# Kernel tuning notes

Measured on AMD Instinct MI355X. Metric: run time of the kernel, lower is better.

Reference implementation:

```python
import jax, jax.numpy as jnp
import numpy as np

DEPTH = 9            # perfect binary tree depth (root=level 0, leaves=level DEPTH)
N_TREES = 128
H = 256              # h_size == x_size (ndata['h'] init uses x_size)
NPT = 2 ** (DEPTH + 1) - 1   # 1023 nodes per tree
N = N_TREES * NPT            # 130944 total nodes


def _levels():
    """Static per-level (node, left-child, right-child) global index arrays."""
    base = np.arange(N_TREES, dtype=np.int64)[:, None] * NPT
    out = []
    for l in range(DEPTH + 1):
        loc = np.arange(2 ** l - 1, 2 ** (l + 1) - 1, dtype=np.int64)
        nodes = (base + loc[None, :]).reshape(-1)
        if l < DEPTH:
            cl = (base + (2 * loc + 1)[None, :]).reshape(-1)
            cr = (base + (2 * loc + 2)[None, :]).reshape(-1)
        else:
            cl = cr = None
        out.append((jnp.asarray(nodes),
                    None if cl is None else jnp.asarray(cl),
                    None if cr is None else jnp.asarray(cr)))
    return out


def setup_inputs() -> dict:
    key = jax.random.key(0)
    ks = jax.random.split(key, 10)
    s = lambda d: 1.0 / np.sqrt(d)
    return {
        "wordid": jax.random.randint(ks[0], (N,), 0, 32000),
        "mask":   jax.random.randint(ks[1], (N,), 0, 2),
        "emb":    jax.random.normal(ks[2], (32000, H), jnp.float32) * 0.02,
        "W_iou":  jax.random.normal(ks[3], (H, 3 * H), jnp.float32) * s(H),
        "U_iou":  jax.random.normal(ks[4], (2 * H, 3 * H), jnp.float32) * s(2 * H),
        "U_f_w":  jax.random.normal(ks[5], (2 * H, 2 * H), jnp.float32) * s(2 * H),
        "U_f_b":  jax.random.normal(ks[6], (2 * H,), jnp.float32) * 0.01,
        "b_iou":  jax.random.normal(ks[7], (3 * H,), jnp.float32) * 0.01,
        "lin_w":  jax.random.normal(ks[8], (H, 4), jnp.float32) * s(H),
        "lin_b":  jax.random.normal(ks[9], (4,), jnp.float32) * 0.01,
    }


def _apply_node(iou, b_iou, c_in, mh_in):
    i, o, u = jnp.split(iou + b_iou, 3, axis=1)
    i, o, u = jax.nn.sigmoid(i), jax.nn.sigmoid(o), jnp.tanh(u)
    c = i * u + c_in
    h = o * jnp.tanh(c)
    return h, c, jnp.maximum(h, mh_in)


def reference(wordid, mask, emb, W_iou, U_iou, U_f_w, U_f_b, b_iou, lin_w, lin_b):
    levels = _levels()
    x = emb[wordid * mask]                                  # [N, H]
    iou0 = (x @ W_iou) * mask[:, None].astype(x.dtype)      # leaf/pre-set iou [N, 3H]

    h = jnp.zeros((N, H), x.dtype)
    c = jnp.zeros((N, H), x.dtype)
    mh = jnp.zeros((N, H), x.dtype)

    # leaves: no incoming messages -> apply with preset iou, c=0, max_h=0
    li, _, _ = levels[DEPTH]
    hh, cc, mm = _apply_node(iou0[li], b_iou, 0.0, 0.0)
    h, c, mh = h.at[li].set(hh), c.at[li].set(cc), mh.at[li].set(mm)

    # internal levels, bottom-up (DGL prop_nodes_topo)
    for l in range(DEPTH - 1, -1, -1):
        ni, cl, cr = levels[l]
        h_cat = jnp.concatenate([h[cl], h[cr]], axis=1)     # [M, 2H]
        f = jax.nn.sigmoid(h_cat @ U_f_w + U_f_b)           # [M, 2H]
        fl, fr = jnp.split(f, 2, axis=1)
        c_red = fl * c[cl] + fr * c[cr]
        mh_red = jnp.maximum(mh[cl], mh[cr])
        iou = h_cat @ U_iou                                  # overwrites preset iou
        hh, cc, mm = _apply_node(iou, b_iou, c_red, mh_red)
        h, c, mh = h.at[ni].set(hh), c.at[ni].set(cc), mh.at[ni].set(mm)

    return (h + mh) @ lin_w + lin_b                         # logits [N, num_classes]
```

## Files before the change

kernel.cpp:

```cpp
#include <hip/hip_runtime.h>
#include <hip/hip_bf16.h>


#define NTREES 128
#define NPT    1023
#define HS     256
#define NNODES (NTREES * NPT)
#define NL     (NTREES * 512)

typedef __hip_bfloat16 bf16;
typedef unsigned short us8 __attribute__((ext_vector_type(8)));
typedef unsigned short us4 __attribute__((ext_vector_type(4)));
typedef short bf16x8 __attribute__((ext_vector_type(8)));
typedef float f32x4 __attribute__((ext_vector_type(4)));

typedef __attribute__((address_space(1))) const void gvoid;
typedef __attribute__((address_space(3))) void svoid;
#define GLD16(gp, lp) \
    __builtin_amdgcn_global_load_lds((gvoid*)(gp), (svoid*)(lp), 16, 0, 0)

__device__ __forceinline__ float bits2f(unsigned short b) {
    return __uint_as_float(((unsigned)b) << 16);
}
__device__ __forceinline__ unsigned short f2bits(float x) {
    bf16 h = __float2bfloat16(x);
    return *reinterpret_cast<unsigned short*>(&h);
}
__device__ __forceinline__ float fsigm(float x) {
    return __builtin_amdgcn_rcpf(1.0f + __expf(-x));
}
__device__ __forceinline__ float ftanh(float x) {
    return 1.0f - 2.0f * __builtin_amdgcn_rcpf(1.0f + __expf(2.0f * x));
}

#define WT_ELEMS (768 * 256)
#define UT_ELEMS (1280 * 512)

__global__ __launch_bounds__(256) void prep_w(
    const float* __restrict__ W_iou, const float* __restrict__ U_f_w,
    const float* __restrict__ U_iou, bf16* __restrict__ Wt, bf16* __restrict__ Ut)
{
    const int i = blockIdx.x * 256 + threadIdx.x;
    if (i < WT_ELEMS) {
        const int n = i >> 8, k = i & 255;
        Wt[i] = __float2bfloat16(W_iou[k * 768 + n]);
    } else if (i < WT_ELEMS + UT_ELEMS) {
        const int j = i - WT_ELEMS;
        const int n = j >> 9, k = j & 511;
        const float v = (n < 512) ? U_f_w[k * 512 + n] : U_iou[k * 768 + (n - 512)];
        Ut[j] = __float2bfloat16(v);
    }
}

__global__ __launch_bounds__(256) void gather_x(
    const int* __restrict__ wordid, const int* __restrict__ mask,
    const float* __restrict__ emb, bf16* __restrict__ x_bf)
{
    const int wave = threadIdx.x >> 6, lane = threadIdx.x & 63;
    const int gr   = blockIdx.x * 4 + wave;
    const int node = (gr >> 9) * NPT + 511 + (gr & 511);
    const int j0   = lane * 4;
    us4 v;
    if (mask[node]) {
        const float4 f = *(const float4*)(emb + (long)wordid[node] * HS + j0);
        v[0] = f2bits(f.x); v[1] = f2bits(f.y);
        v[2] = f2bits(f.z); v[3] = f2bits(f.w);
    } else {
        v[0] = v[1] = v[2] = v[3] = 0;
    }
    *(us4*)(x_bf + (long)gr * HS + j0) = v;
}

__global__ __launch_bounds__(256) void leaf_fused(
    const bf16* __restrict__ x_bf, const bf16* __restrict__ Wt,
    const float* __restrict__ b_iou,
    bf16* __restrict__ h_s, bf16* __restrict__ cm_s,
    bf16* __restrict__ s_full, const int tree0)
{
    __shared__ __align__(16) short a_s[2][128 * 32];
    __shared__ __align__(16) short b_s[2][128 * 32];
    const int t    = threadIdx.x;
    const int bm0  = blockIdx.x * 128;
    const int c0   = blockIdx.y * 32;
    const int lane = t & 63, wave = t >> 6;
    const int l4a = lane >> 2, k8 = (lane & 3) * 8;

    const bf16* aSrc[2];
    #pragma unroll
    for (int q = 0; q < 2; ++q) {
        const int row = (wave * 2 + q) * 16 + l4a;
        aSrc[q] = x_bf + (long)(tree0 * 512 + bm0 + row) * HS + k8;
    }
    const bf16* bSrc[2];
    #pragma unroll
    for (int q = 0; q < 2; ++q) {
        int rb = (wave * 2 + q) * 16 + l4a;
        if (rb > 95) rb = 95;
        const int g = rb >> 5, jl = rb & 31;
        bSrc[q] = Wt + (long)(g * 256 + c0 + jl) * 256 + k8;
    }

    const int wr = wave >> 1, wc = wave & 1;
    const int fr = lane & 15, l4 = lane >> 4;

    f32x4 acc[4][3];
    #pragma unroll
    for (int i = 0; i < 4; ++i)
        #pragma unroll
        for (int g = 0; g < 3; ++g) acc[i][g] = (f32x4){0.f, 0.f, 0.f, 0.f};

    auto stage = [&](int buf, int step) {
        const int kt = step * 32;
        #pragma unroll
        for (int q = 0; q < 2; ++q)
            GLD16(aSrc[q] + kt, &a_s[buf][(wave * 2 + q) * 512]);
        #pragma unroll
        for (int q = 0; q < 2; ++q)
            GLD16(bSrc[q] + kt, &b_s[buf][(wave * 2 + q) * 512]);
    };

    stage(0, 0);
    stage(1, 1);
    int cur = 0;
    for (int it = 0; it < 8; ++it) {
        if (it < 7) { asm volatile("s_waitcnt vmcnt(4)" ::: "memory"); }
        else        { asm volatile("s_waitcnt vmcnt(0)" ::: "memory"); }
        __builtin_amdgcn_sched_barrier(0);
        __builtin_amdgcn_s_barrier();
        __builtin_amdgcn_sched_barrier(0);
        bf16x8 af[4], bg[3];
        #pragma unroll
        for (int i = 0; i < 4; ++i)
            af[i] = *(const bf16x8*)&a_s[cur][(wr * 64 + i * 16 + fr) * 32 + l4 * 8];
        #pragma unroll
        for (int g = 0; g < 3; ++g)
            bg[g] = *(const bf16x8*)&b_s[cur][(g * 32 + wc * 16 + fr) * 32 + l4 * 8];
        #pragma unroll
        for (int i = 0; i < 4; ++i)
            #pragma unroll
            for (int g = 0; g < 3; ++g)
                acc[i][g] = __builtin_amdgcn_mfma_f32_16x16x32_bf16(
                    bg[g], af[i], acc[i][g], 0, 0, 0);
        __builtin_amdgcn_s_barrier();
        __builtin_amdgcn_sched_barrier(0);
        if (it < 6) stage(cur, it + 2);
        cur ^= 1;
    }

    const int j0 = c0 + wc * 16 + l4 * 4;
    const float4 bi4 = *(const float4*)(b_iou + j0);
    const float4 bo4 = *(const float4*)(b_iou + 256 + j0);
    const float4 bu4 = *(const float4*)(b_iou + 512 + j0);
    #pragma unroll
    for (int i = 0; i < 4; ++i) {
        const int r    = bm0 + wr * 64 + i * 16 + fr;
        const int gr   = tree0 * 512 + r;
        const int node = (gr >> 9) * NPT + 511 + (gr & 511);
        us4 sh, ss; us8 scm;
        #pragma unroll
        for (int q = 0; q < 4; ++q) {
            const float iv = fsigm(acc[i][0][q] + ((const float*)&bi4)[q]);
            const float ov = fsigm(acc[i][1][q] + ((const float*)&bo4)[q]);
            const float uv = ftanh(acc[i][2][q] + ((const float*)&bu4)[q]);
            const float cv  = iv * uv;
            const float hv  = ov * ftanh(cv);
            const float mhv = fmaxf(hv, 0.0f);
            sh[q] = f2bits(hv); ss[q] = f2bits(hv + mhv);
            scm[2 * q] = f2bits(cv); scm[2 * q + 1] = f2bits(mhv);
        }
        *(us4*)(h_s + (long)r * HS + j0)        = sh;
        *(us8*)(cm_s + (long)r * 512 + j0 * 2)  = scm;
        *(us4*)(s_full + (long)node * HS + j0)  = ss;
    }
}

__global__ __launch_bounds__(256) void level_fused(
    const bf16* __restrict__ h_child, const bf16* __restrict__ cm_c,
    const bf16* __restrict__ Ut,
    const float* __restrict__ U_f_b, const float* __restrict__ b_iou,
    bf16* __restrict__ h_p, bf16* __restrict__ cm_p,
    bf16* __restrict__ s_full, const int lvl, const int M, const int tree0)
{
    __shared__ __align__(16) short a_s[2][128 * 32];
    __shared__ __align__(16) short b_s[2][192 * 32];
    const int t    = threadIdx.x;
    const int bm0  = blockIdx.x * 128;
    const int c0   = blockIdx.y * 32;
    const int lane = t & 63, wave = t >> 6;
    const int l4a = lane >> 2, k8 = (lane & 3) * 8;

    const bf16* aSrc[2];
    #pragma unroll
    for (int q = 0; q < 2; ++q) {
        int p = bm0 + (wave * 2 + q) * 16 + l4a;
        if (p >= M) p = M - 1;
        const int tl  = p >> lvl;
        const int idx = p & ((1 << lvl) - 1);
        const int cls = tl * (2 << lvl) + 2 * idx;
        aSrc[q] = h_child + (long)cls * HS + k8;
    }
    const bf16* bSrc[3];
    #pragma unroll
    for (int q = 0; q < 3; ++q) {
        int rb = (wave * 3 + q) * 16 + l4a;
        if (rb > 159) rb = 159;
        const int g = rb >> 5, jl = rb & 31;
        bSrc[q] = Ut + (long)(g * 256 + c0 + jl) * 512 + k8;
    }

    const int wr = wave >> 1, wc = wave & 1;
    const int fr = lane & 15, l4 = lane >> 4;

    f32x4 acc[4][5];
    #pragma unroll
    for (int i = 0; i < 4; ++i)
        #pragma unroll
        for (int g = 0; g < 5; ++g) acc[i][g] = (f32x4){0.f, 0.f, 0.f, 0.f};

    auto stage = [&](int buf, int step) {
        const int kt = step * 32;
        #pragma unroll
        for (int q = 0; q < 2; ++q)
            GLD16(aSrc[q] + kt, &a_s[buf][(wave * 2 + q) * 512]);
        #pragma unroll
        for (int q = 0; q < 3; ++q)
            GLD16(bSrc[q] + kt, &b_s[buf][(wave * 3 + q) * 512]);
    };

    stage(0, 0);
    stage(1, 1);
    int cur = 0;
    for (int it = 0; it < 16; ++it) {
        if (it < 15) { asm volatile("s_waitcnt vmcnt(5)" ::: "memory"); }
        else         { asm volatile("s_waitcnt vmcnt(0)" ::: "memory"); }
        __builtin_amdgcn_sched_barrier(0);
        __builtin_amdgcn_s_barrier();
        __builtin_amdgcn_sched_barrier(0);
        bf16x8 af[4], bg[5];
        #pragma unroll
        for (int i = 0; i < 4; ++i)
            af[i] = *(const bf16x8*)&a_s[cur][(wr * 64 + i * 16 + fr) * 32 + l4 * 8];
        #pragma unroll
        for (int g = 0; g < 5; ++g)
            bg[g] = *(const bf16x8*)&b_s[cur][(g * 32 + wc * 16 + fr) * 32 + l4 * 8];
        #pragma unroll
        for (int i = 0; i < 4; ++i)
            #pragma unroll
            for (int g = 0; g < 5; ++g)
                acc[i][g] = __builtin_amdgcn_mfma_f32_16x16x32_bf16(
                    bg[g], af[i], acc[i][g], 0, 0, 0);
        __builtin_amdgcn_s_barrier();
        __builtin_amdgcn_sched_barrier(0);
        if (it < 14) stage(cur, it + 2);
        cur ^= 1;
    }

    const int j0 = c0 + wc * 16 + l4 * 4;
    const float4 bfl4 = *(const float4*)(U_f_b + j0);
    const float4 bfr4 = *(const float4*)(U_f_b + 256 + j0);
    const float4 bi4  = *(const float4*)(b_iou + j0);
    const float4 bo4  = *(const float4*)(b_iou + 256 + j0);
    const float4 bu4  = *(const float4*)(b_iou + 512 + j0);
    #pragma unroll
    for (int i = 0; i < 4; ++i) {
        const int r  = bm0 + wr * 64 + i * 16 + fr;
        const int rc = r < M ? r : M - 1;
        const int tl   = rc >> lvl;
        const int idx  = rc & ((1 << lvl) - 1);
        const int cls  = tl * (2 << lvl) + 2 * idx;
        const int node = (tree0 + tl) * NPT + (1 << lvl) - 1 + idx;
        const us8 cml = *(const us8*)(cm_c + (long)cls * 512 + j0 * 2);
        const us8 cmr = *(const us8*)(cm_c + (long)(cls + 1) * 512 + j0 * 2);
        us4 sh, ss; us8 scm;
        #pragma unroll
        for (int q = 0; q < 4; ++q) {
            const float flv = fsigm(acc[i][0][q] + ((const float*)&bfl4)[q]);
            const float frv = fsigm(acc[i][1][q] + ((const float*)&bfr4)[q]);
            const float iv  = fsigm(acc[i][2][q] + ((const float*)&bi4)[q]);
            const float ov  = fsigm(acc[i][3][q] + ((const float*)&bo4)[q]);
            const float uv  = ftanh(acc[i][4][q] + ((const float*)&bu4)[q]);
            const float ccl = bits2f(cml[2 * q]), mhl = bits2f(cml[2 * q + 1]);
            const float ccr = bits2f(cmr[2 * q]), mhr = bits2f(cmr[2 * q + 1]);
            const float cv  = iv * uv + flv * ccl + frv * ccr;
            const float hv  = ov * ftanh(cv);
            const float mhv = fmaxf(hv, fmaxf(mhl, mhr));
            sh[q] = f2bits(hv); ss[q] = f2bits(hv + mhv);
            scm[2 * q] = f2bits(cv); scm[2 * q + 1] = f2bits(mhv);
        }
        if (r < M) {
            *(us4*)(h_p + (long)r * HS + j0)       = sh;
            *(us8*)(cm_p + (long)r * 512 + j0 * 2) = scm;
            *(us4*)(s_full + (long)node * HS + j0) = ss;
        }
    }
}

__global__ __launch_bounds__(256) void logits_k(
    const bf16* __restrict__ s_full, const float* __restrict__ lin_w,
    const float* __restrict__ lin_b, float* __restrict__ out)
{
    const int wave = threadIdx.x >> 6, lane = threadIdx.x & 63;
    const int node = blockIdx.x * 4 + wave;
    const int j0   = lane * 4;
    const us4 v = *(const us4*)(s_full + (long)node * HS + j0);
    float p0 = 0.f, p1 = 0.f, p2 = 0.f, p3 = 0.f;
    #pragma unroll
    for (int q = 0; q < 4; ++q) {
        const float s  = bits2f(v[q]);
        const float4 w = *(const float4*)(lin_w + (j0 + q) * 4);
        p0 += s * w.x; p1 += s * w.y; p2 += s * w.z; p3 += s * w.w;
    }
    #pragma unroll
    for (int m = 1; m < 64; m <<= 1) {
        p0 += __shfl_xor(p0, m); p1 += __shfl_xor(p1, m);
        p2 += __shfl_xor(p2, m); p3 += __shfl_xor(p3, m);
    }
    if (lane == 0) {
        float4 r;
        r.x = p0 + lin_b[0]; r.y = p1 + lin_b[1];
        r.z = p2 + lin_b[2]; r.w = p3 + lin_b[3];
        *(float4*)(out + (long)node * 4) = r;
    }
}

extern "C" void kernel_launch(void* const* d_in, const int* in_sizes, int n_in,
                              void* d_out, int out_size, void* d_ws, size_t ws_size,
                              hipStream_t stream) {
    const int*   wordid = (const int*)d_in[0];
    const int*   mask   = (const int*)d_in[1];
    const float* emb    = (const float*)d_in[2];
    const float* W_iou  = (const float*)d_in[3];
    const float* U_iou  = (const float*)d_in[4];
    const float* U_f_w  = (const float*)d_in[5];
    const float* U_f_b  = (const float*)d_in[6];
    const float* b_iou  = (const float*)d_in[7];
    const float* lin_w  = (const float*)d_in[8];
    const float* lin_b  = (const float*)d_in[9];
    float* out = (float*)d_out;

    const size_t wElems = (size_t)WT_ELEMS + UT_ELEMS;
    const size_t sElems = (size_t)NNODES * HS;
    const size_t xElems = (size_t)NL * HS;
    auto need = [&](int T) -> size_t {
        return (wElems + sElems + xElems + (size_t)T * 589824) * 2;
    };
    int T = 8;
    const int cands[4] = {128, 64, 32, 16};
    for (int ci = 0; ci < 4; ++ci) {
        if (need(cands[ci]) <= ws_size) { T = cands[ci]; break; }
    }

    bf16* Wt     = (bf16*)d_ws;
    bf16* Ut     = Wt + WT_ELEMS;
    bf16* s_full = Ut + UT_ELEMS;
    bf16* x_bf   = s_full + sElems;
    bf16* hA  = x_bf + xElems;
    bf16* cmA = hA  + (size_t)T * 512 * HS;
    bf16* hB  = cmA + (size_t)T * 512 * HS * 2;
    bf16* cmB = hB  + (size_t)T * 256 * HS;

    prep_w<<<(int)((wElems + 255) / 256), 256, 0, stream>>>(
        W_iou, U_f_w, U_iou, Wt, Ut);
    gather_x<<<NL / 4, 256, 0, stream>>>(wordid, mask, emb, x_bf);

    for (int tree0 = 0; tree0 < NTREES; tree0 += T) {
        leaf_fused<<<dim3(T * 512 / 128, 8), 256, 0, stream>>>(
            x_bf, Wt, b_iou, hA, cmA, s_full, tree0);
        bool childIsA = true;
        for (int l = 8; l >= 0; --l) {
            bf16 *hc, *cmc, *hp, *cmp;
            if (childIsA) { hc = hA; cmc = cmA; hp = hB; cmp = cmB; }
            else          { hc = hB; cmc = cmB; hp = hA; cmp = cmA; }
            const int M = T << l;
            level_fused<<<dim3((M + 127) / 128, 8), 256, 0, stream>>>(
                hc, cmc, Ut, U_f_b, b_iou, hp, cmp, s_full, l, M, tree0);
            childIsA = !childIsA;
        }
    }
    logits_k<<<NNODES / 4, 256, 0, stream>>>(s_full, lin_w, lin_b, out);
}
```

Before: 426.7 us.

## Load weight fragments directly into registers instead of staging through LDS

In both the leaf and level GEMM kernels, the B (weight) operand is no longer staged through shared memory. Each wave now issues direct global loads of its MFMA B fragments into double-buffered registers (even/odd), and only the A operand keeps LDS staging via global_load_lds. This removes the LDS writes and reads and shrinks shared memory use, which could raise occupancy. In exchange it adds VGPR pressure, and weight loads are redundant across the wr wave pairs instead of shared cooperatively.

```diff
diff --git a/kernel.cpp b/kernel.cpp
--- a/kernel.cpp
+++ b/kernel.cpp
@@ -18,6 +18,8 @@
 typedef __attribute__((address_space(3))) void svoid;
 #define GLD16(gp, lp) \
     __builtin_amdgcn_global_load_lds((gvoid*)(gp), (svoid*)(lp), 16, 0, 0)
+#define SBAR()  __builtin_amdgcn_s_barrier()
+#define SCHED() __builtin_amdgcn_sched_barrier(0)
 
 __device__ __forceinline__ float bits2f(unsigned short b) {
     return __uint_as_float(((unsigned)b) << 16);
@@ -78,30 +80,25 @@
     bf16* __restrict__ s_full, const int tree0)
 {
     __shared__ __align__(16) short a_s[2][128 * 32];
-    __shared__ __align__(16) short b_s[2][128 * 32];
     const int t    = threadIdx.x;
     const int bm0  = blockIdx.x * 128;
     const int c0   = blockIdx.y * 32;
     const int lane = t & 63, wave = t >> 6;
     const int l4a = lane >> 2, k8 = (lane & 3) * 8;
 
+    const int wr = wave >> 1, wc = wave & 1;
+    const int fr = lane & 15, l4 = lane >> 4;
+
     const bf16* aSrc[2];
     #pragma unroll
     for (int q = 0; q < 2; ++q) {
         const int row = (wave * 2 + q) * 16 + l4a;
         aSrc[q] = x_bf + (long)(tree0 * 512 + bm0 + row) * HS + k8;
     }
-    const bf16* bSrc[2];
-    #pragma unroll
-    for (int q = 0; q < 2; ++q) {
-        int rb = (wave * 2 + q) * 16 + l4a;
-        if (rb > 95) rb = 95;
-        const int g = rb >> 5, jl = rb & 31;
-        bSrc[q] = Wt + (long)(g * 256 + c0 + jl) * 256 + k8;
-    }
-
-    const int wr = wave >> 1, wc = wave & 1;
-    const int fr = lane & 15, l4 = lane >> 4;
+    const bf16* bPtr[3];
+    #pragma unroll
+    for (int g = 0; g < 3; ++g)
+        bPtr[g] = Wt + (long)(g * 256 + c0 + wc * 16 + fr) * 256 + l4 * 8;
 
     f32x4 acc[4][3];
     #pragma unroll
@@ -109,42 +106,52 @@
         #pragma unroll
         for (int g = 0; g < 3; ++g) acc[i][g] = (f32x4){0.f, 0.f, 0.f, 0.f};
 
-    auto stage = [&](int buf, int step) {
-        const int kt = step * 32;
-        #pragma unroll
-        for (int q = 0; q < 2; ++q)
-            GLD16(aSrc[q] + kt, &a_s[buf][(wave * 2 + q) * 512]);
-        #pragma unroll
-        for (int q = 0; q < 2; ++q)
-            GLD16(bSrc[q] + kt, &b_s[buf][(wave * 2 + q) * 512]);
-    };
-
-    stage(0, 0);
-    stage(1, 1);
-    int cur = 0;
+    bf16x8 bgE[3], bgO[3];
+
+    #pragma unroll
+    for (int q = 0; q < 2; ++q) GLD16(aSrc[q], &a_s[0][(wave * 2 + q) * 512]);
+    SCHED();
+    #pragma unroll
+    for (int g = 0; g < 3; ++g) bgE[g] = *(const bf16x8*)(bPtr[g]);
+    SCHED();
+    #pragma unroll
+    for (int q = 0; q < 2; ++q) GLD16(aSrc[q] + 32, &a_s[1][(wave * 2 + q) * 512]);
+    SCHED();
+    #pragma unroll
+    for (int g = 0; g < 3; ++g) bgO[g] = *(const bf16x8*)(bPtr[g] + 32);
+    SCHED();
+
+    #pragma unroll
     for (int it = 0; it < 8; ++it) {
-        if (it < 7) { asm volatile("s_waitcnt vmcnt(4)" ::: "memory"); }
+        const int cur = it & 1;
+        if (it < 7) { asm volatile("s_waitcnt vmcnt(5)" ::: "memory"); }
         else        { asm volatile("s_waitcnt vmcnt(0)" ::: "memory"); }
-        __builtin_amdgcn_sched_barrier(0);
-        __builtin_amdgcn_s_barrier();
-        __builtin_amdgcn_sched_barrier(0);
-        bf16x8 af[4], bg[3];
+        SCHED(); SBAR(); SCHED();
+        bf16x8 af[4];
         #pragma unroll
         for (int i = 0; i < 4; ++i)
             af[i] = *(const bf16x8*)&a_s[cur][(wr * 64 + i * 16 + fr) * 32 + l4 * 8];
         #pragma unroll
-        for (int g = 0; g < 3; ++g)
-            bg[g] = *(const bf16x8*)&b_s[cur][(g * 32 + wc * 16 + fr) * 32 + l4 * 8];
-        #pragma unroll
         for (int i = 0; i < 4; ++i)
             #pragma unroll
             for (int g = 0; g < 3; ++g)
                 acc[i][g] = __builtin_amdgcn_mfma_f32_16x16x32_bf16(
-                    bg[g], af[i], acc[i][g], 0, 0, 0);
-        __builtin_amdgcn_s_barrier();
-        __builtin_amdgcn_sched_barrier(0);
-        if (it < 6) stage(cur, it + 2);
-        cur ^= 1;
+                    cur ? bgO[g] : bgE[g], af[i], acc[i][g], 0, 0, 0);
+        SCHED();
+        if (it + 2 < 8) {
+            #pragma unroll
+            for (int g = 0; g < 3; ++g) {
+                if (cur) bgO[g] = *(const bf16x8*)(bPtr[g] + (it + 2) * 32);
+                else     bgE[g] = *(const bf16x8*)(bPtr[g] + (it + 2) * 32);
+            }
+        }
+        SCHED(); SBAR(); SCHED();
+        if (it + 2 < 8) {
+            #pragma unroll
+            for (int q = 0; q < 2; ++q)
+                GLD16(aSrc[q] + (it + 2) * 32, &a_s[cur][(wave * 2 + q) * 512]);
+        }
+        SCHED();
     }
 
     const int j0 = c0 + wc * 16 + l4 * 4;
@@ -182,12 +189,14 @@
     bf16* __restrict__ s_full, const int lvl, const int M, const int tree0)
 {
     __shared__ __align__(16) short a_s[2][128 * 32];
-    __shared__ __align__(16) short b_s[2][192 * 32];
     const int t    = threadIdx.x;
     const int bm0  = blockIdx.x * 128;
     const int c0   = blockIdx.y * 32;
     const int lane = t & 63, wave = t >> 6;
     const int l4a = lane >> 2, k8 = (lane & 3) * 8;
+
+    const int wr = wave >> 1, wc = wave & 1;
+    const int fr = lane & 15, l4 = lane >> 4;
 
     const bf16* aSrc[2];
     #pragma unroll
@@ -199,17 +208,10 @@
         const int cls = tl * (2 << lvl) + 2 * idx;
         aSrc[q] = h_child + (long)cls * HS + k8;
     }
-    const bf16* bSrc[3];
-    #pragma unroll
-    for (int q = 0; q < 3; ++q) {
-        int rb = (wave * 3 + q) * 16 + l4a;
-        if (rb > 159) rb = 159;
-        const int g = rb >> 5, jl = rb & 31;
-        bSrc[q] = Ut + (long)(g * 256 + c0 + jl) * 512 + k8;
-    }
-
-    const int wr = wave >> 1, wc = wave & 1;
-    const int fr = lane & 15, l4 = lane >> 4;
+    const bf16* bPtr[5];
+    #pragma unroll
+    for (int g = 0; g < 5; ++g)
+        bPtr[g] = Ut + (long)(g * 256 + c0 + wc * 16 + fr) * 512 + l4 * 8;
 
     f32x4 acc[4][5];
     #pragma unroll
@@ -217,42 +219,52 @@
         #pragma unroll
         for (int g = 0; g < 5; ++g) acc[i][g] = (f32x4){0.f, 0.f, 0.f, 0.f};
 
-    auto stage = [&](int buf, int step) {
-        const int kt = step * 32;
-        #pragma unroll
-        for (int q = 0; q < 2; ++q)
-            GLD16(aSrc[q] + kt, &a_s[buf][(wave * 2 + q) * 512]);
-        #pragma unroll
-        for (int q = 0; q < 3; ++q)
-            GLD16(bSrc[q] + kt, &b_s[buf][(wave * 3 + q) * 512]);
-    };
-
-    stage(0, 0);
-    stage(1, 1);
-    int cur = 0;
+    bf16x8 bgE[5], bgO[5];
+
+    #pragma unroll
+    for (int q = 0; q < 2; ++q) GLD16(aSrc[q], &a_s[0][(wave * 2 + q) * 512]);
+    SCHED();
+    #pragma unroll
+    for (int g = 0; g < 5; ++g) bgE[g] = *(const bf16x8*)(bPtr[g]);
+    SCHED();
+    #pragma unroll
+    for (int q = 0; q < 2; ++q) GLD16(aSrc[q] + 32, &a_s[1][(wave * 2 + q) * 512]);
+    SCHED();
+    #pragma unroll
+    for (int g = 0; g < 5; ++g) bgO[g] = *(const bf16x8*)(bPtr[g] + 32);
+    SCHED();
+
+    #pragma unroll
     for (int it = 0; it < 16; ++it) {
-        if (it < 15) { asm volatile("s_waitcnt vmcnt(5)" ::: "memory"); }
+        const int cur = it & 1;
+        if (it < 15) { asm volatile("s_waitcnt vmcnt(7)" ::: "memory"); }
         else         { asm volatile("s_waitcnt vmcnt(0)" ::: "memory"); }
-        __builtin_amdgcn_sched_barrier(0);
-        __builtin_amdgcn_s_barrier();
-        __builtin_amdgcn_sched_barrier(0);
-        bf16x8 af[4], bg[5];
+        SCHED(); SBAR(); SCHED();
+        bf16x8 af[4];
         #pragma unroll
         for (int i = 0; i < 4; ++i)
             af[i] = *(const bf16x8*)&a_s[cur][(wr * 64 + i * 16 + fr) * 32 + l4 * 8];
         #pragma unroll
-        for (int g = 0; g < 5; ++g)
-            bg[g] = *(const bf16x8*)&b_s[cur][(g * 32 + wc * 16 + fr) * 32 + l4 * 8];
-        #pragma unroll
         for (int i = 0; i < 4; ++i)
             #pragma unroll
             for (int g = 0; g < 5; ++g)
                 acc[i][g] = __builtin_amdgcn_mfma_f32_16x16x32_bf16(
-                    bg[g], af[i], acc[i][g], 0, 0, 0);
-        __builtin_amdgcn_s_barrier();
-        __builtin_amdgcn_sched_barrier(0);
-        if (it < 14) stage(cur, it + 2);
-        cur ^= 1;
+                    cur ? bgO[g] : bgE[g], af[i], acc[i][g], 0, 0, 0);
+        SCHED();
+        if (it + 2 < 16) {
+            #pragma unroll
+            for (int g = 0; g < 5; ++g) {
+                if (cur) bgO[g] = *(const bf16x8*)(bPtr[g] + (it + 2) * 32);
+                else     bgE[g] = *(const bf16x8*)(bPtr[g] + (it + 2) * 32);
+            }
+        }
+        SCHED(); SBAR(); SCHED();
+        if (it + 2 < 16) {
+            #pragma unroll
+            for (int q = 0; q < 2; ++q)
+                GLD16(aSrc[q] + (it + 2) * 32, &a_s[cur][(wave * 2 + q) * 512]);
+        }
+        SCHED();
     }
 
     const int j0 = c0 + wc * 16 + l4 * 4;
```

After: 520.4 us. 1.22x slower.
